# Optimization experiments

Measured on AMD Instinct MI355X. Metric: run time of the kernel, lower is better.

## Reference

```python
import jax, jax.numpy as jnp
import numpy as np
from jax import lax

D_MODEL = 1024
D_INNER = 2048   # expand * d_model
D_STATE = 16
D_CONV = 4
DT_RANK = 64     # ceil(d_model / 16)
B_SZ, L_SEQ = 2, 2048


def setup_inputs() -> dict:
    key = jax.random.key(0)
    ks = jax.random.split(key, 12)
    s = lambda *sh: 1.0 / np.sqrt(sh[-1])
    inp = {
        "x": jax.random.normal(ks[0], (B_SZ, L_SEQ, D_MODEL), jnp.float32),
        "in_proj_w": jax.random.normal(ks[1], (2 * D_INNER, D_MODEL), jnp.float32) * s(D_MODEL),
        "conv_w": jax.random.normal(ks[2], (D_INNER, 1, D_CONV), jnp.float32) * 0.3,
        "conv_b": jax.random.normal(ks[3], (D_INNER,), jnp.float32) * 0.05,
        "x_proj_w": jax.random.normal(ks[4], (DT_RANK + 2 * D_STATE, D_INNER), jnp.float32) * s(D_INNER),
        "dt_proj_w": jax.random.normal(ks[5], (D_INNER, DT_RANK), jnp.float32) * s(DT_RANK),
        "dt_proj_b": jnp.log(jnp.exp(jax.random.uniform(ks[6], (D_INNER,), jnp.float32, 1e-3, 1e-1)) - 1.0),
        "A_log": jnp.log(jnp.broadcast_to(jnp.arange(1, D_STATE + 1, dtype=jnp.float32), (D_INNER, D_STATE))),
        "D": jnp.ones((D_INNER,), jnp.float32),
        "out_proj_w": jax.random.normal(ks[7], (D_MODEL, D_INNER), jnp.float32) * s(D_INNER),
        "ln_w": jnp.ones((D_MODEL,), jnp.float32),
        "ln_b": jnp.zeros((D_MODEL,), jnp.float32),
    }
    return inp


def _mamba(x, in_proj_w, conv_w, conv_b, x_proj_w, dt_proj_w, dt_proj_b, A_log, D, out_proj_w):
    # x: [B, L, d_model]
    xz = x @ in_proj_w.T                             # [B, L, 2*d_inner]
    u, z = jnp.split(xz, 2, axis=-1)                 # [B, L, d_inner] each
    # depthwise causal conv1d along L
    u_c = jnp.swapaxes(u, 1, 2)                      # [B, d_inner, L]
    u_c = lax.conv_general_dilated(
        u_c, conv_w, window_strides=(1,), padding=[(D_CONV - 1, 0)],
        feature_group_count=D_INNER, dimension_numbers=("NCH", "OIH", "NCH"))
    u_c = u_c + conv_b[None, :, None]
    u_c = jax.nn.silu(jnp.swapaxes(u_c, 1, 2))       # [B, L, d_inner]
    # input-dependent dt, B, C
    x_dbl = u_c @ x_proj_w.T                         # [B, L, dt_rank + 2*d_state]
    dt_lr = x_dbl[..., :DT_RANK]
    Bm = x_dbl[..., DT_RANK:DT_RANK + D_STATE]       # [B, L, d_state]
    Cm = x_dbl[..., DT_RANK + D_STATE:]              # [B, L, d_state]
    dt = jax.nn.softplus(dt_lr @ dt_proj_w.T + dt_proj_b)  # [B, L, d_inner]
    A = -jnp.exp(A_log)                              # [d_inner, d_state]

    def step(h, inputs):
        dt_t, b_t, c_t, u_t = inputs                 # [B,d_inner],[B,N],[B,N],[B,d_inner]
        dA = jnp.exp(dt_t[:, :, None] * A)           # [B, d_inner, N]
        h = h * dA + (dt_t * u_t)[:, :, None] * b_t[:, None, :]
        y_t = jnp.einsum("bdn,bn->bd", h, c_t)
        return h, y_t

    h0 = jnp.zeros((x.shape[0], D_INNER, D_STATE), x.dtype)
    xs = (jnp.swapaxes(dt, 0, 1), jnp.swapaxes(Bm, 0, 1),
          jnp.swapaxes(Cm, 0, 1), jnp.swapaxes(u_c, 0, 1))
    _, ys = lax.scan(step, h0, xs)                   # ys: [L, B, d_inner]
    y = jnp.swapaxes(ys, 0, 1) + u_c * D             # skip connection D*u
    y = y * jax.nn.silu(z)                           # gate
    return y @ out_proj_w.T                          # [B, L, d_model]


def _layernorm(x, w, b, eps=1e-5):
    mu = jnp.mean(x, axis=-1, keepdims=True)
    var = jnp.mean(jnp.square(x - mu), axis=-1, keepdims=True)
    return (x - mu) * lax.rsqrt(var + eps) * w + b


def reference(x, in_proj_w, conv_w, conv_b, x_proj_w, dt_proj_w, dt_proj_b,
              A_log, D, out_proj_w, ln_w, ln_b):
    y = _mamba(x, in_proj_w, conv_w, conv_b, x_proj_w, dt_proj_w, dt_proj_b,
               A_log, D, out_proj_w)
    return _layernorm(y + x, ln_w, ln_b)  # dropout_level=0 -> identity
```

## Files before the change

### kernel.cpp

```cpp
#include <hip/hip_runtime.h>
#include <hip/hip_bf16.h>
#include <math.h>

#define DEV static __device__ __forceinline__

typedef __hip_bfloat16 bf16;
typedef __attribute__((ext_vector_type(8))) short bf16x8;
typedef __attribute__((ext_vector_type(4))) short bf16x4;
typedef __attribute__((ext_vector_type(4))) float f32x4;

static constexpr int D_MODEL = 1024;
static constexpr int D_INNER = 2048;
static constexpr int D_STATE = 16;
static constexpr int DT_RANK = 64;
static constexpr int B_SZ   = 2;
static constexpr int L_SEQ  = 2048;
static constexpr int T_TOK  = B_SZ * L_SEQ;
static constexpr int LC     = 64;
static constexpr int NC     = L_SEQ / LC;
static constexpr int NXP    = DT_RANK + 2 * D_STATE;
static constexpr int KSPLIT = 8;

static constexpr int P_CONVW = 0;
static constexpr int P_CONVB = 8192;
static constexpr int P_DTB   = 10240;
static constexpr int P_ALOG  = 12288;
static constexpr int P_DW    = 45056;
static constexpr int P_LNW   = 47104;
static constexpr int P_LNB   = 48128;
static constexpr int P_TOT   = 49152;

DEV float bf2f(bf16 x) { return __bfloat162float(x); }
DEV bf16  f2bf(float x) { return __float2bfloat16(x); }
DEV float sigmoidf_(float x) { return 1.0f / (1.0f + __expf(-x)); }
DEV float s2f(short s) { bf16 b; __builtin_memcpy(&b, &s, 2); return bf2f(b); }
DEV short f2s(float x) { bf16 b = f2bf(x); short s; __builtin_memcpy(&s, &b, 2); return s; }

DEV bool probe_f32(const unsigned short* probe) { return probe[1] == 0; }

DEV void async_copy16(const void* g, void* l) {
  __builtin_amdgcn_global_load_lds(
      (const __attribute__((address_space(1))) void*)g,
      (__attribute__((address_space(3))) void*)l, 16, 0, 0);
}

template <int N>
DEV void vm_wait() {
  if constexpr (N == 6) asm volatile("s_waitcnt vmcnt(6)" ::: "memory");
  else                  asm volatile("s_waitcnt vmcnt(0)" ::: "memory");
}

__global__ void cvt_all(const void* s0, const void* s1, const void* s2,
                        const void* s3, const void* s4,
                        const void* s5, const void* s6, const void* s7,
                        const void* s8, const void* s9, const void* s10,
                        const void* s11,
                        bf16* d0, bf16* d1, bf16* d2, bf16* d3, bf16* d4,
                        float* params,
                        const unsigned short* __restrict__ probe)
{
  long i = (long)(blockIdx.x * 256 + threadIdx.x) * 8;
  const void* src; long off;
  bf16* dstb = nullptr; float* dstf = nullptr;
  if      (i <  4194304) { src = s0;  dstb = d0; off = i; }
  else if (i <  8388608) { src = s1;  dstb = d1; off = i - 4194304; }
  else if (i <  8585216) { src = s2;  dstb = d2; off = i - 8388608; }
  else if (i <  8716288) { src = s3;  dstb = d3; off = i - 8585216; }
  else if (i < 10813440) { src = s4;  dstb = d4; off = i - 8716288; }
  else if (i < 10821632) { src = s5;  dstf = params + P_CONVW; off = i - 10813440; }
  else if (i < 10823680) { src = s6;  dstf = params + P_CONVB; off = i - 10821632; }
  else if (i < 10825728) { src = s7;  dstf = params + P_DTB;   off = i - 10823680; }
  else if (i < 10858496) { src = s8;  dstf = params + P_ALOG;  off = i - 10825728; }
  else if (i < 10860544) { src = s9;  dstf = params + P_DW;    off = i - 10858496; }
  else if (i < 10861568) { src = s10; dstf = params + P_LNW;   off = i - 10860544; }
  else if (i < 10862592) { src = s11; dstf = params + P_LNB;   off = i - 10861568; }
  else return;
  bool isf32 = probe_f32(probe);
  float v[8];
  if (isf32) {
    float4 a = *(const float4*)((const float*)src + off);
    float4 b = *(const float4*)((const float*)src + off + 4);
    v[0]=a.x; v[1]=a.y; v[2]=a.z; v[3]=a.w;
    v[4]=b.x; v[5]=b.y; v[6]=b.z; v[7]=b.w;
  } else {
    bf16x8 t = *(const bf16x8*)((const bf16*)src + off);
    #pragma unroll
    for (int k = 0; k < 8; ++k) { short sk = t[k]; v[k] = s2f(sk); }
  }
  if (dstb) {
    bf16x8 o;
    #pragma unroll
    for (int k = 0; k < 8; ++k) o[k] = f2s(v[k]);
    *(bf16x8*)(dstb + off) = o;
  } else {
    f32x4 a = {v[0], v[1], v[2], v[3]};
    f32x4 b = {v[4], v[5], v[6], v[7]};
    *(f32x4*)(dstf + off)     = a;
    *(f32x4*)(dstf + off + 4) = b;
  }
}

static constexpr int SLOT = 48 * 1024;
static constexpr int BOFF = 32 * 1024;

DEV void stage_A(const bf16* __restrict__ A, int ld, int bm, int k0,
                 char* slot, int tid) {
  #pragma unroll
  for (int j = 0; j < 4; ++j) {
    int p   = j * 8192 + tid * 16;
    int row = p >> 7;
    int ck  = ((p >> 4) & 7) ^ (row & 7);
    async_copy16(A + (size_t)(bm + row) * ld + k0 + ck * 8,
                 slot + j * 8192 + (tid >> 6) * 1024);
  }
}

DEV void stage_B(const bf16* __restrict__ B, int ld, int bn, int k0,
                 char* slot, int tid) {
  #pragma unroll
  for (int j = 0; j < 2; ++j) {
    int p   = j * 8192 + tid * 16;
    int row = p >> 7;
    int ck  = ((p >> 4) & 7) ^ (row & 7);
    async_copy16(B + (size_t)(bn + row) * ld + k0 + ck * 8,
                 slot + BOFF + j * 8192 + (tid >> 6) * 1024);
  }
}

template <int MODE>
DEV void gemm_pipe(const bf16* __restrict__ A, const bf16* __restrict__ B,
                   int M, int K, int ld,
                   void* __restrict__ o0, void* __restrict__ o1,
                   const float* __restrict__ cw, const float* __restrict__ cb)
{
  __shared__ __align__(16) char ring[3 * SLOT];
  const bf16* Aorig = A;
  const bf16* Borig = B;
  if (MODE == 3) {
    A += (size_t)blockIdx.z * K;
    B += (size_t)blockIdx.z * K;
  }
  const int tid  = threadIdx.x;
  const int wave = tid >> 6;
  const int lane = tid & 63;
  const int bm = blockIdx.x * 256;
  const int bn = blockIdx.y * 128;
  const int wm = (wave >> 1) * 64;
  const int wn = (wave & 1) * 64;
  const int fr = lane & 15;
  const int fq = lane >> 4;
  const int NT = K / 64;

  f32x4 acc[4][4];
  #pragma unroll
  for (int i = 0; i < 4; ++i)
    #pragma unroll
    for (int j = 0; j < 4; ++j)
      #pragma unroll
      for (int r = 0; r < 4; ++r) acc[i][j][r] = 0.0f;

  stage_A(A, ld, bm, 0,  ring,        tid);
  stage_B(B, ld, bn, 0,  ring,        tid);
  stage_A(A, ld, bm, 64, ring + SLOT, tid);
  stage_B(B, ld, bn, 64, ring + SLOT, tid);

  int scur = 0;
  #pragma unroll 1
  for (int tk = 0; tk < NT; ++tk) {
    if (tk < NT - 1) vm_wait<6>();
    else             vm_wait<0>();
    __builtin_amdgcn_sched_barrier(0);
    __builtin_amdgcn_s_barrier();
    __builtin_amdgcn_sched_barrier(0);

    const char* sa = ring + scur * SLOT;
    int snxt = scur + 2; if (snxt >= 3) snxt -= 3;
    char* sn = ring + snxt * SLOT;

    bf16x8 af[4][2], bg[2][2];
    #pragma unroll
    for (int mi = 0; mi < 4; ++mi)
      #pragma unroll
      for (int kk = 0; kk < 2; ++kk) {
        int row = wm + mi * 16 + fr;
        af[mi][kk] = *(const bf16x8*)(sa + row * 128 + (((kk * 4 + fq) ^ (fr & 7)) * 16));
      }
    #pragma unroll
    for (int ni = 0; ni < 2; ++ni)
      #pragma unroll
      for (int kk = 0; kk < 2; ++kk) {
        int row = wn + ni * 16 + fr;
        bg[ni][kk] = *(const bf16x8*)(sa + BOFF + row * 128 + (((kk * 4 + fq) ^ (fr & 7)) * 16));
      }
    __builtin_amdgcn_sched_barrier(0);
    if (tk + 2 < NT) stage_A(A, ld, bm, (tk + 2) * 64, sn, tid);
    __builtin_amdgcn_sched_barrier(0);
    asm volatile("s_waitcnt lgkmcnt(0)" ::: "memory");
    __builtin_amdgcn_sched_barrier(0);
    __builtin_amdgcn_s_setprio(1);
    #pragma unroll
    for (int kk = 0; kk < 2; ++kk)
      #pragma unroll
      for (int mi = 0; mi < 4; ++mi)
        #pragma unroll
        for (int ni = 0; ni < 2; ++ni)
          acc[mi][ni] = __builtin_amdgcn_mfma_f32_16x16x32_bf16(af[mi][kk], bg[ni][kk], acc[mi][ni], 0, 0, 0);
    __builtin_amdgcn_s_setprio(0);
    __builtin_amdgcn_sched_barrier(0);

    bf16x8 bh[2][2];
    #pragma unroll
    for (int ni = 0; ni < 2; ++ni)
      #pragma unroll
      for (int kk = 0; kk < 2; ++kk) {
        int row = wn + (ni + 2) * 16 + fr;
        bh[ni][kk] = *(const bf16x8*)(sa + BOFF + row * 128 + (((kk * 4 + fq) ^ (fr & 7)) * 16));
      }
    __builtin_amdgcn_sched_barrier(0);
    if (tk + 2 < NT) stage_B(B, ld, bn, (tk + 2) * 64, sn, tid);
    __builtin_amdgcn_sched_barrier(0);
    asm volatile("s_waitcnt lgkmcnt(0)" ::: "memory");
    __builtin_amdgcn_sched_barrier(0);
    __builtin_amdgcn_s_setprio(1);
    #pragma unroll
    for (int kk = 0; kk < 2; ++kk)
      #pragma unroll
      for (int mi = 0; mi < 4; ++mi)
        #pragma unroll
        for (int ni = 0; ni < 2; ++ni)
          acc[mi][ni + 2] = __builtin_amdgcn_mfma_f32_16x16x32_bf16(af[mi][kk], bh[ni][kk], acc[mi][ni + 2], 0, 0, 0);
    __builtin_amdgcn_s_setprio(0);
    __builtin_amdgcn_sched_barrier(0);

    scur = (scur + 1 == 3) ? 0 : scur + 1;
  }

  const int er = (lane >> 4) * 4;
  const int ec = lane & 15;

  if (MODE == 3) {
    #pragma unroll
    for (int mi = 0; mi < 4; ++mi)
      #pragma unroll
      for (int ni = 0; ni < 4; ++ni)
        #pragma unroll
        for (int r = 0; r < 4; ++r) {
          int row = bm + wm + mi * 16 + er + r;
          int col = bn + wn + ni * 16 + ec;
          ((bf16*)o0)[((size_t)blockIdx.z * M + row) * D_MODEL + col] = f2bf(acc[mi][ni][r]);
        }
    return;
  }

  if (bn >= D_INNER) {
    #pragma unroll
    for (int mi = 0; mi < 4; ++mi)
      #pragma unroll
      for (int ni = 0; ni < 4; ++ni)
        #pragma unroll
        for (int r = 0; r < 4; ++r) {
          int row = bm + wm + mi * 16 + er + r;
          int col = bn + wn + ni * 16 + ec - D_INNER;
          float v = acc[mi][ni][r];
          ((bf16*)o1)[(size_t)row * D_INNER + col] = f2bf(v * sigmoidf_(v));
        }
    return;
  }

  __syncthreads();
  bf16*  uT  = (bf16*)ring;
  float* cws = (float*)(ring + 70656);
  float* cbs = (float*)(ring + 72704);

  #pragma unroll
  for (int mi = 0; mi < 4; ++mi)
    #pragma unroll
    for (int ni = 0; ni < 4; ++ni)
      #pragma unroll
      for (int r = 0; r < 4; ++r)
        uT[(size_t)(wm + mi * 16 + er + r + 3) * 136 + wn + ni * 16 + ec] = f2bf(acc[mi][ni][r]);

  if (tid < 128) {
    *(f32x4*)(cws + tid * 4) = *(const f32x4*)(cw + (size_t)(bn + tid) * 4);
    cbs[tid] = cb[bn + tid];
  }

  if ((bm & (L_SEQ - 1)) != 0 && tid < 384) {
    int j = tid >> 7;
    int c = tid & 127;
    const bf16* xr = Aorig + (size_t)(bm - 3 + j) * ld;
    const bf16* wr = Borig + (size_t)(bn + c) * ld;
    float s = 0.0f;
    for (int k8 = 0; k8 < 1024; k8 += 8) {
      bf16x8 xa = *(const bf16x8*)(xr + k8);
      bf16x8 wb = *(const bf16x8*)(wr + k8);
      #pragma unroll
      for (int q = 0; q < 8; ++q) { short a = xa[q], b = wb[q]; s += s2f(a) * s2f(b); }
    }
    uT[(size_t)j * 136 + c] = f2bf(s);
  }
  __syncthreads();

  const int cg = tid & 15;
  float cwr[4][8], cbr[8];
  #pragma unroll
  for (int i = 0; i < 8; ++i) {
    f32x4 w4 = *(const f32x4*)(cws + (cg * 8 + i) * 4);
    cwr[0][i] = w4[0]; cwr[1][i] = w4[1]; cwr[2][i] = w4[2]; cwr[3][i] = w4[3];
    cbr[i] = cbs[cg * 8 + i];
  }
  const int lbase = bm & (L_SEQ - 1);
  #pragma unroll
  for (int j = 0; j < 8; ++j) {
    int row = (tid >> 4) + j * 32;
    float a8[8];
    #pragma unroll
    for (int i = 0; i < 8; ++i) a8[i] = cbr[i];
    #pragma unroll
    for (int w = 0; w < 4; ++w) {
      if (lbase + row - 3 + w >= 0) {
        bf16x8 u8 = *(const bf16x8*)(uT + (size_t)(row + w) * 136 + cg * 8);
        #pragma unroll
        for (int i = 0; i < 8; ++i) { short uu = u8[i]; a8[i] += s2f(uu) * cwr[w][i]; }
      }
    }
    bf16x8 o;
    #pragma unroll
    for (int i = 0; i < 8; ++i) o[i] = f2s(a8[i] * sigmoidf_(a8[i]));
    *(bf16x8*)((bf16*)o0 + (size_t)(bm + row) * D_INNER + bn + cg * 8) = o;
  }
}

__global__ void __launch_bounds__(256) k_xproj(const bf16* __restrict__ A,
                                               const bf16* __restrict__ B,
                                               float* __restrict__ o0)
{
  __shared__ __align__(16) bf16 As[128 * 32];
  __shared__ __align__(16) bf16 Bs[128 * 32];
  const int M = T_TOK, N = NXP, K = D_INNER / KSPLIT, ld = D_INNER;
  A += (size_t)blockIdx.z * K;
  B += (size_t)blockIdx.z * K;
  const int tid  = threadIdx.x;
  const int wave = tid >> 6;
  const int lane = tid & 63;
  const int bm = blockIdx.x * 128;
  const int bn = 0;
  const int wm = (wave >> 1) * 64;
  const int wn = (wave & 1) * 64;

  f32x4 acc[4][4];
  #pragma unroll
  for (int i = 0; i < 4; ++i)
    #pragma unroll
    for (int j = 0; j < 4; ++j)
      #pragma unroll
      for (int r = 0; r < 4; ++r) acc[i][j][r] = 0.0f;

  const int ar0 = tid >> 2;
  const int ar1 = ar0 + 64;
  const int ac  = (tid & 3) * 8;
  const int fr = lane & 15;
  const int fk = (lane >> 4) * 8;

  for (int k0 = 0; k0 < K; k0 += 32) {
    bf16x8 a0 = *(const bf16x8*)(A + (size_t)(bm + ar0) * ld + k0 + ac);
    bf16x8 a1 = *(const bf16x8*)(A + (size_t)(bm + ar1) * ld + k0 + ac);
    int r0 = bn + ar0; if (r0 > N - 1) r0 = N - 1;
    int r1 = bn + ar1; if (r1 > N - 1) r1 = N - 1;
    bf16x8 b0 = *(const bf16x8*)(B + (size_t)r0 * ld + k0 + ac);
    bf16x8 b1 = *(const bf16x8*)(B + (size_t)r1 * ld + k0 + ac);
    __syncthreads();
    *(bf16x8*)(As + ar0 * 32 + ac) = a0;
    *(bf16x8*)(As + ar1 * 32 + ac) = a1;
    *(bf16x8*)(Bs + ar0 * 32 + ac) = b0;
    *(bf16x8*)(Bs + ar1 * 32 + ac) = b1;
    __syncthreads();

    bf16x8 af[4], bg[4];
    #pragma unroll
    for (int mi = 0; mi < 4; ++mi)
      af[mi] = *(const bf16x8*)(As + (wm + mi * 16 + fr) * 32 + fk);
    #pragma unroll
    for (int ni = 0; ni < 4; ++ni)
      bg[ni] = *(const bf16x8*)(Bs + (wn + ni * 16 + fr) * 32 + fk);
    #pragma unroll
    for (int mi = 0; mi < 4; ++mi)
      #pragma unroll
      for (int ni = 0; ni < 4; ++ni)
        acc[mi][ni] = __builtin_amdgcn_mfma_f32_16x16x32_bf16(af[mi], bg[ni], acc[mi][ni], 0, 0, 0);
  }

  const int er = (lane >> 4) * 4;
  const int ec = lane & 15;
  #pragma unroll
  for (int mi = 0; mi < 4; ++mi)
    #pragma unroll
    for (int ni = 0; ni < 4; ++ni)
      #pragma unroll
      for (int r = 0; r < 4; ++r) {
        int row = bm + wm + mi * 16 + er + r;
        int col = bn + wn + ni * 16 + ec;
        if (col >= N) continue;
        o0[((size_t)blockIdx.z * M + row) * N + col] = acc[mi][ni][r];
      }
}

__global__ void __launch_bounds__(512) k_inproj(const bf16* A, const bf16* B,
    void* o0, void* o1, const float* cw, const float* cb) {
  gemm_pipe<0>(A, B, T_TOK, D_MODEL, D_MODEL, o0, o1, cw, cb);
}
__global__ void __launch_bounds__(512) k_outproj(const bf16* A, const bf16* B,
    void* o0) {
  gemm_pipe<3>(A, B, T_TOK, D_INNER / 2, D_INNER, o0, nullptr, nullptr, nullptr);
}

__global__ __launch_bounds__(256) void k_dtfuse(
    const float* __restrict__ partials,
    const bf16*  __restrict__ dtw,
    const float* __restrict__ dtbias,
    float* __restrict__ Bbuf, float* __restrict__ Cbuf,
    bf16* __restrict__ dtb)
{
  __shared__ __align__(16) bf16 Al[128 * 72];
  __shared__ __align__(16) bf16 Bl[128 * 72];
  const int tid = threadIdx.x;
  unsigned lin = blockIdx.x + gridDim.x * blockIdx.y;
  unsigned nid = (lin & 7) * 64 + (lin >> 3);
  const int cblk = nid & 15;
  const int tblk = nid >> 4;
  const int r0 = tblk * 128;
  const int c0 = cblk * 128;

  #pragma unroll
  for (int it = 0; it < 8; ++it) {
    int idx = it * 256 + tid;
    int row = idx >> 4;
    int g   = idx & 15;
    f32x4 s = {0.0f, 0.0f, 0.0f, 0.0f};
    #pragma unroll
    for (int kz = 0; kz < KSPLIT; ++kz)
      s += *(const f32x4*)(partials + ((size_t)kz * T_TOK + r0 + row) * NXP + g * 4);
    bf16x4 o;
    #pragma unroll
    for (int k = 0; k < 4; ++k) o[k] = f2s(s[k]);
    *(bf16x4*)(Al + row * 72 + g * 4) = o;
  }
  if (cblk == 0) {
    #pragma unroll
    for (int it = 0; it < 4; ++it) {
      int idx = it * 256 + tid;
      int row = idx >> 3;
      int g   = 16 + (idx & 7);
      f32x4 s = {0.0f, 0.0f, 0.0f, 0.0f};
      #pragma unroll
      for (int kz = 0; kz < KSPLIT; ++kz)
        s += *(const f32x4*)(partials + ((size_t)kz * T_TOK + r0 + row) * NXP + g * 4);
      if (g < 20) *(f32x4*)(Bbuf + (size_t)(r0 + row) * D_STATE + (g - 16) * 4) = s;
      else        *(f32x4*)(Cbuf + (size_t)(r0 + row) * D_STATE + (g - 20) * 4) = s;
    }
  }
  #pragma unroll
  for (int it = 0; it < 4; ++it) {
    int idx = it * 256 + tid;
    int row = idx >> 3;
    int cv  = (idx & 7) * 8;
    *(bf16x8*)(Bl + row * 72 + cv) = *(const bf16x8*)(dtw + (size_t)(c0 + row) * 64 + cv);
  }
  __syncthreads();

  const int wave = tid >> 6;
  const int lane = tid & 63;
  const int wm = (wave >> 1) * 64;
  const int wn = (wave & 1) * 64;
  const int fr = lane & 15;
  const int fk = (lane >> 4) * 8;
  const int er = (lane >> 4) * 4;
  const int ec = lane & 15;

  f32x4 acc[4][4];
  #pragma unroll
  for (int i = 0; i < 4; ++i)
    #pragma unroll
    for (int j = 0; j < 4; ++j)
      #pragma unroll
      for (int r = 0; r < 4; ++r) acc[i][j][r] = 0.0f;

  #pragma unroll
  for (int k0 = 0; k0 < 64; k0 += 32) {
    bf16x8 af[4], bg[4];
    #pragma unroll
    for (int mi = 0; mi < 4; ++mi)
      af[mi] = *(const bf16x8*)(Al + (wm + mi * 16 + fr) * 72 + k0 + fk);
    #pragma unroll
    for (int ni = 0; ni < 4; ++ni)
      bg[ni] = *(const bf16x8*)(Bl + (wn + ni * 16 + fr) * 72 + k0 + fk);
    #pragma unroll
    for (int mi = 0; mi < 4; ++mi)
      #pragma unroll
      for (int ni = 0; ni < 4; ++ni)
        acc[mi][ni] = __builtin_amdgcn_mfma_f32_16x16x32_bf16(af[mi], bg[ni], acc[mi][ni], 0, 0, 0);
  }

  #pragma unroll
  for (int mi = 0; mi < 4; ++mi)
    #pragma unroll
    for (int ni = 0; ni < 4; ++ni)
      #pragma unroll
      for (int r = 0; r < 4; ++r) {
        int orow = r0 + wm + mi * 16 + er + r;
        int ocol = c0 + wn + ni * 16 + ec;
        float v = acc[mi][ni][r] + dtbias[ocol];
        float sp = (v > 15.0f) ? v : __logf(1.0f + __expf(v));
        dtb[(size_t)orow * D_INNER + ocol] = f2bf(sp);
      }
}

DEV void load_Ad(const float* A_log, int d, float* Ad, bool& fast) {
  fast = true;
  #pragma unroll
  for (int n = 0; n < 16; ++n) {
    Ad[n] = -__expf(A_log[d * 16 + n]);
    fast = fast && (fabsf(Ad[n] + (float)(n + 1)) < 1e-3f * (n + 1));
  }
}
DEV void compute_decay(bool fast, float dtv, const float* Ad, float* dec) {
  if (fast) {
    float e1 = __expf(-dtv);
    float en = e1;
    #pragma unroll
    for (int n = 0; n < 16; ++n) { dec[n] = en; en *= e1; }
  } else {
    #pragma unroll
    for (int n = 0; n < 16; ++n) dec[n] = __expf(Ad[n] * dtv);
  }
}

__global__ __launch_bounds__(256) void scan_pass1(
    const bf16* __restrict__ dt, const bf16* __restrict__ uc_bf,
    const float* __restrict__ Bbuf, const float* __restrict__ A_log,
    float* __restrict__ hend, float* __restrict__ sumdt)
{
  __shared__ float Bs4[LC * D_STATE];
  __shared__ bf16 dts[16 * 256];
  __shared__ bf16 uts[16 * 256];
  int bid = blockIdx.x;
  int tid = threadIdx.x;
  int dt8 = bid & 7;
  int c = (bid >> 3) & (NC - 1);
  int b = bid >> 8;
  int d0 = dt8 * 256;
  int d  = d0 + tid;
  int t0g = b * L_SEQ + c * LC;

  ((f32x4*)Bs4)[tid] = ((const f32x4*)(Bbuf + (size_t)t0g * D_STATE))[tid];

  float Ad[16], h[16];
  bool fast;
  load_Ad(A_log, d, Ad, fast);
  #pragma unroll
  for (int n = 0; n < 16; ++n) h[n] = 0.0f;
  float sdt = 0.0f;

  for (int sub = 0; sub < 4; ++sub) {
    __syncthreads();
    #pragma unroll
    for (int rep = 0; rep < 2; ++rep) {
      int idx = rep * 256 + tid;
      int row = idx >> 5;
      int col = (idx & 31) * 8;
      size_t src = (size_t)(t0g + sub * 16 + row) * D_INNER + d0 + col;
      *(bf16x8*)(dts + row * 256 + col) = *(const bf16x8*)(dt + src);
      *(bf16x8*)(uts + row * 256 + col) = *(const bf16x8*)(uc_bf + src);
    }
    __syncthreads();
    for (int t = 0; t < 16; ++t) {
      float dtv = bf2f(dts[t * 256 + tid]);
      float uv  = bf2f(uts[t * 256 + tid]);
      float su  = dtv * uv;
      sdt += dtv;
      float dec[16];
      compute_decay(fast, dtv, Ad, dec);
      const float* Bp = Bs4 + (sub * 16 + t) * 16;
      #pragma unroll
      for (int n = 0; n < 16; ++n)
        h[n] = h[n] * dec[n] + su * Bp[n];
    }
  }
  size_t base = ((size_t)(b * NC + c) * D_INNER + d) * 16;
  #pragma unroll
  for (int q = 0; q < 4; ++q)
    *(f32x4*)(hend + base + q * 4) = *(f32x4*)(h + q * 4);
  sumdt[(size_t)(b * NC + c) * D_INNER + d] = sdt;
}

__global__ __launch_bounds__(256) void scan_pass2(
    float* __restrict__ hend, const float* __restrict__ sumdt,
    const float* __restrict__ A_log)
{
  __shared__ float Ms[4][64];
  __shared__ float Es[4][64];
  int bid = blockIdx.x;
  int tid = threadIdx.x;
  int cg   = tid >> 6;
  int lane = tid & 63;
  int dloc = lane >> 4;
  int n    = lane & 15;
  int b     = bid >> 9;
  int d     = (bid & 511) * 4 + dloc;

  float a = -__expf(A_log[d * 16 + n]);

  float Ml[8], El[8];
  float M = 1.0f, E = 0.0f;
  #pragma unroll
  for (int j = 0; j < 8; ++j) {
    int c = cg * 8 + j;
    size_t sbase = (size_t)(b * NC + c) * D_INNER + d;
    float m = __expf(a * sumdt[sbase]);
    float e = hend[sbase * 16 + n];
    Ml[j] = M; El[j] = E;
    M = m * M;
    E = m * E + e;
  }
  Ms[cg][lane] = M;
  Es[cg][lane] = E;
  __syncthreads();
  float Ep = 0.0f;
  for (int g = 0; g < cg; ++g) {
    float Mg = Ms[g][lane], Eg = Es[g][lane];
    Ep = Mg * Ep + Eg;
  }
  #pragma unroll
  for (int j = 0; j < 8; ++j) {
    int c = cg * 8 + j;
    size_t sbase = (size_t)(b * NC + c) * D_INNER + d;
    hend[sbase * 16 + n] = Ml[j] * Ep + El[j];
  }
}

__global__ __launch_bounds__(256) void scan_pass3(
    const bf16* __restrict__ dt, const bf16* __restrict__ uc_bf,
    const float* __restrict__ Bbuf, const float* __restrict__ Cbuf,
    const bf16* __restrict__ z_silu, const float* __restrict__ hstart,
    const float* __restrict__ A_log, const float* __restrict__ Dw,
    bf16* __restrict__ y_bf)
{
  __shared__ float Bs4[LC * D_STATE];
  __shared__ float Cs4[LC * D_STATE];
  __shared__ bf16 dts[16 * 256];
  __shared__ bf16 uts[16 * 256];
  __shared__ bf16 zts[16 * 256];
  int bid = blockIdx.x;
  int tid = threadIdx.x;
  int dt8 = bid & 7;
  int c = (bid >> 3) & (NC - 1);
  int b = bid >> 8;
  int d0 = dt8 * 256;
  int d  = d0 + tid;
  int t0g = b * L_SEQ + c * LC;

  ((f32x4*)Bs4)[tid] = ((const f32x4*)(Bbuf + (size_t)t0g * D_STATE))[tid];
  ((f32x4*)Cs4)[tid] = ((const f32x4*)(Cbuf + (size_t)t0g * D_STATE))[tid];

  float Ad[16], h[16];
  bool fast;
  load_Ad(A_log, d, Ad, fast);
  size_t base = ((size_t)(b * NC + c) * D_INNER + d) * 16;
  #pragma unroll
  for (int q = 0; q < 4; ++q)
    *(f32x4*)(h + q * 4) = *(const f32x4*)(hstart + base + q * 4);
  float Dv = Dw[d];

  for (int sub = 0; sub < 4; ++sub) {
    __syncthreads();
    #pragma unroll
    for (int rep = 0; rep < 2; ++rep) {
      int idx = rep * 256 + tid;
      int row = idx >> 5;
      int col = (idx & 31) * 8;
      size_t src = (size_t)(t0g + sub * 16 + row) * D_INNER + d0 + col;
      *(bf16x8*)(dts + row * 256 + col) = *(const bf16x8*)(dt + src);
      *(bf16x8*)(uts + row * 256 + col) = *(const bf16x8*)(uc_bf + src);
      *(bf16x8*)(zts + row * 256 + col) = *(const bf16x8*)(z_silu + src);
    }
    __syncthreads();
    for (int t = 0; t < 16; ++t) {
      float dtv = bf2f(dts[t * 256 + tid]);
      float uv  = bf2f(uts[t * 256 + tid]);
      float zv  = bf2f(zts[t * 256 + tid]);
      float su  = dtv * uv;
      float dec[16];
      compute_decay(fast, dtv, Ad, dec);
      const float* Bp = Bs4 + (sub * 16 + t) * 16;
      const float* Cp = Cs4 + (sub * 16 + t) * 16;
      float y = 0.0f;
      #pragma unroll
      for (int n = 0; n < 16; ++n) {
        h[n] = h[n] * dec[n] + su * Bp[n];
        y += h[n] * Cp[n];
      }
      y = (y + uv * Dv) * zv;
      y_bf[(size_t)(t0g + sub * 16 + t) * D_INNER + d] = f2bf(y);
    }
  }
}

__global__ void ln_kernel(const bf16* __restrict__ parts,
                          const bf16* __restrict__ x_bf,
                          const float* __restrict__ w,
                          const float* __restrict__ bia,
                          void* __restrict__ out,
                          const unsigned short* __restrict__ probe)
{
  int t = blockIdx.x;
  int tid = threadIdx.x;
  const bf16* p0 = parts + (size_t)t * D_MODEL;
  const bf16* p1 = parts + ((size_t)T_TOK + t) * D_MODEL;
  const bf16* xr = x_bf + (size_t)t * D_MODEL;
  float v[4];
  float s = 0.0f, q = 0.0f;
  #pragma unroll
  for (int k = 0; k < 4; ++k) {
    int col = tid + k * 256;
    v[k] = bf2f(p0[col]) + bf2f(p1[col]) + bf2f(xr[col]);
    s += v[k]; q += v[k] * v[k];
  }
  #pragma unroll
  for (int off = 32; off >= 1; off >>= 1) {
    s += __shfl_down(s, off);
    q += __shfl_down(q, off);
  }
  __shared__ float red[8];
  __shared__ float mv[2];
  int wave = tid >> 6, lane = tid & 63;
  if (lane == 0) { red[wave] = s; red[4 + wave] = q; }
  __syncthreads();
  if (tid == 0) {
    float S = red[0] + red[1] + red[2] + red[3];
    float Q = red[4] + red[5] + red[6] + red[7];
    float mu = S * (1.0f / D_MODEL);
    float var = Q * (1.0f / D_MODEL) - mu * mu;
    mv[0] = mu; mv[1] = rsqrtf(var + 1e-5f);
  }
  __syncthreads();
  float mu = mv[0], rs = mv[1];
  bool isf32 = probe_f32(probe);
  #pragma unroll
  for (int k = 0; k < 4; ++k) {
    int col = tid + k * 256;
    float r = (v[k] - mu) * rs * w[col] + bia[col];
    if (isf32) ((float*)out)[(size_t)t * D_MODEL + col] = r;
    else       ((bf16*) out)[(size_t)t * D_MODEL + col] = f2bf(r);
  }
}

extern "C" void kernel_launch(void* const* d_in, const int* in_sizes, int n_in,
                              void* d_out, int out_size, void* d_ws, size_t ws_size,
                              hipStream_t stream)
{
  const void* x        = d_in[0];
  const void* in_w     = d_in[1];
  const void* conv_w   = d_in[2];
  const void* conv_b   = d_in[3];
  const void* xproj_w  = d_in[4];
  const void* dtproj_w = d_in[5];
  const void* dtproj_b = d_in[6];
  const void* A_log    = d_in[7];
  const void* Dw       = d_in[8];
  const void* out_w    = d_in[9];
  const void* ln_w     = d_in[10];
  const void* ln_b     = d_in[11];
  const unsigned short* probe = (const unsigned short*)A_log;

  char* p = (char*)d_ws;
  auto alloc = [&](size_t bytes) { char* r = p; p += (bytes + 255) & ~255ull; return r; };
  bf16*  x_bf   = (bf16*) alloc((size_t)T_TOK * D_MODEL * 2);
  bf16*  inw_bf = (bf16*) alloc((size_t)2 * D_INNER * D_MODEL * 2);
  bf16*  xpw_bf = (bf16*) alloc((size_t)NXP * D_INNER * 2);
  bf16*  dtw_bf = (bf16*) alloc((size_t)D_INNER * DT_RANK * 2);
  bf16*  outw_bf= (bf16*) alloc((size_t)D_MODEL * D_INNER * 2);
  float* params = (float*)alloc((size_t)P_TOT * 4);
  bf16*  scratch= (bf16*) alloc((size_t)T_TOK * D_INNER * 2);
  bf16*  z_silu = (bf16*) alloc((size_t)T_TOK * D_INNER * 2);
  bf16*  uc_bf  = (bf16*) alloc((size_t)T_TOK * D_INNER * 2);
  float* Bbuf   = (float*)alloc((size_t)T_TOK * D_STATE * 4);
  float* Cbuf   = (float*)alloc((size_t)T_TOK * D_STATE * 4);
  bf16*  dtb    = (bf16*) alloc((size_t)T_TOK * D_INNER * 2);
  float* hend   = (float*)alloc((size_t)B_SZ * NC * D_INNER * 16 * 4);
  float* sumdt  = (float*)alloc((size_t)B_SZ * NC * D_INNER * 4);
  float* xparts = (float*)scratch;
  bf16*  y_bf   = scratch;
  bf16*  oparts = z_silu;

  dim3 blk(256);
  dim3 blk512(512);
  cvt_all<<<5304, blk, 0, stream>>>(x, in_w, xproj_w, dtproj_w, out_w,
                                    conv_w, conv_b, dtproj_b, A_log, Dw, ln_w, ln_b,
                                    x_bf, inw_bf, xpw_bf, dtw_bf, outw_bf, params, probe);

  k_inproj<<<dim3(T_TOK / 256, (2 * D_INNER) / 128), blk512, 0, stream>>>(
      x_bf, inw_bf, uc_bf, z_silu, params + P_CONVW, params + P_CONVB);
  k_xproj<<<dim3(T_TOK / 128, 1, KSPLIT), blk, 0, stream>>>(uc_bf, xpw_bf, xparts);
  k_dtfuse<<<dim3(16, 32), blk, 0, stream>>>(xparts, dtw_bf, params + P_DTB, Bbuf, Cbuf, dtb);
  scan_pass1<<<B_SZ * NC * (D_INNER / 256), blk, 0, stream>>>(dtb, uc_bf, Bbuf, params + P_ALOG, hend, sumdt);
  scan_pass2<<<(B_SZ * D_INNER) / 2, blk, 0, stream>>>(hend, sumdt, params + P_ALOG);
  scan_pass3<<<B_SZ * NC * (D_INNER / 256), blk, 0, stream>>>(
      dtb, uc_bf, Bbuf, Cbuf, z_silu, hend, params + P_ALOG, params + P_DW, y_bf);
  k_outproj<<<dim3(T_TOK / 256, D_MODEL / 128, 2), blk512, 0, stream>>>(y_bf, outw_bf, oparts);
  ln_kernel<<<T_TOK, blk, 0, stream>>>(oparts, x_bf, params + P_LNW, params + P_LNB, d_out, probe);
}
```

Before: 294.6 us.

## Replace in-GEMM halo recomputation with cross-tile boundary exchange and fixup kernel

Before, each in_proj tile recomputed the three preceding token rows of u with a scalar 1024-long dot product, so the depthwise conv had its causal halo. That serial per-thread loop ran in the GEMM epilogue. Now each tile writes its first and last three u rows to small global buffers and skips the first three conv outputs. A new small kernel then recomputes those boundary conv outputs from the neighbouring tiles' rows. This removes the slow scalar halo work from the GEMM, at the cost of one extra tiny kernel launch and its dependency.

```diff
diff --git a/kernel.cpp b/kernel.cpp
--- a/kernel.cpp
+++ b/kernel.cpp
@@ -131,11 +131,10 @@
 DEV void gemm_pipe(const bf16* __restrict__ A, const bf16* __restrict__ B,
                    int M, int K, int ld,
                    void* __restrict__ o0, void* __restrict__ o1,
-                   const float* __restrict__ cw, const float* __restrict__ cb)
+                   const float* __restrict__ cw, const float* __restrict__ cb,
+                   bf16* __restrict__ ufirst, bf16* __restrict__ ulast)
 {
   __shared__ __align__(16) char ring[3 * SLOT];
-  const bf16* Aorig = A;
-  const bf16* Borig = B;
   if (MODE == 3) {
     A += (size_t)blockIdx.z * K;
     B += (size_t)blockIdx.z * K;
@@ -278,28 +277,21 @@
     for (int ni = 0; ni < 4; ++ni)
       #pragma unroll
       for (int r = 0; r < 4; ++r)
-        uT[(size_t)(wm + mi * 16 + er + r + 3) * 136 + wn + ni * 16 + ec] = f2bf(acc[mi][ni][r]);
+        uT[(size_t)(wm + mi * 16 + er + r) * 136 + wn + ni * 16 + ec] = f2bf(acc[mi][ni][r]);
 
   if (tid < 128) {
     *(f32x4*)(cws + tid * 4) = *(const f32x4*)(cw + (size_t)(bn + tid) * 4);
     cbs[tid] = cb[bn + tid];
   }
-
-  if ((bm & (L_SEQ - 1)) != 0 && tid < 384) {
-    int j = tid >> 7;
-    int c = tid & 127;
-    const bf16* xr = Aorig + (size_t)(bm - 3 + j) * ld;
-    const bf16* wr = Borig + (size_t)(bn + c) * ld;
-    float s = 0.0f;
-    for (int k8 = 0; k8 < 1024; k8 += 8) {
-      bf16x8 xa = *(const bf16x8*)(xr + k8);
-      bf16x8 wb = *(const bf16x8*)(wr + k8);
-      #pragma unroll
-      for (int q = 0; q < 8; ++q) { short a = xa[q], b = wb[q]; s += s2f(a) * s2f(b); }
-    }
-    uT[(size_t)j * 136 + c] = f2bf(s);
-  }
   __syncthreads();
+
+  if (tid < 48) {
+    int i  = tid >> 4;
+    int c8 = (tid & 15) * 8;
+    size_t hb = ((size_t)(bm >> 8) * 3 + i) * D_INNER + bn + c8;
+    *(bf16x8*)(ufirst + hb) = *(const bf16x8*)(uT + (size_t)i * 136 + c8);
+    *(bf16x8*)(ulast  + hb) = *(const bf16x8*)(uT + (size_t)(253 + i) * 136 + c8);
+  }
 
   const int cg = tid & 15;
   float cwr[4][8], cbr[8];
@@ -313,13 +305,14 @@
   #pragma unroll
   for (int j = 0; j < 8; ++j) {
     int row = (tid >> 4) + j * 32;
+    if (row < 3 && lbase != 0) continue;
     float a8[8];
     #pragma unroll
     for (int i = 0; i < 8; ++i) a8[i] = cbr[i];
     #pragma unroll
     for (int w = 0; w < 4; ++w) {
-      if (lbase + row - 3 + w >= 0) {
-        bf16x8 u8 = *(const bf16x8*)(uT + (size_t)(row + w) * 136 + cg * 8);
+      if (row - 3 + w >= 0) {
+        bf16x8 u8 = *(const bf16x8*)(uT + (size_t)(row - 3 + w) * 136 + cg * 8);
         #pragma unroll
         for (int i = 0; i < 8; ++i) { short uu = u8[i]; a8[i] += s2f(uu) * cwr[w][i]; }
       }
@@ -329,6 +322,41 @@
     for (int i = 0; i < 8; ++i) o[i] = f2s(a8[i] * sigmoidf_(a8[i]));
     *(bf16x8*)((bf16*)o0 + (size_t)(bm + row) * D_INNER + bn + cg * 8) = o;
   }
+}
+
+__global__ void __launch_bounds__(256) k_convfix(
+    const bf16* __restrict__ ufirst, const bf16* __restrict__ ulast,
+    const float* __restrict__ cw, const float* __restrict__ cb,
+    bf16* __restrict__ uc_bf)
+{
+  int idx = blockIdx.x * 256 + threadIdx.x;
+  int e4 = idx * 4;
+  int ti = e4 >> 11;
+  int c4 = e4 & 2047;
+  int tb = ti / 3, r = ti - tb * 3;
+  int rb = (tb < 7) ? tb + 1 : tb + 2;
+  int token = rb * 256 + r;
+  float a[4];
+  float4 wv[4];
+  #pragma unroll
+  for (int i = 0; i < 4; ++i) {
+    a[i]  = cb[c4 + i];
+    wv[i] = *(const float4*)(cw + (size_t)(c4 + i) * 4);
+  }
+  #pragma unroll
+  for (int w = 0; w < 4; ++w) {
+    int g = r - 3 + w;
+    const bf16* srcrow = (g < 0)
+        ? (ulast  + ((size_t)(rb - 1) * 3 + (g + 3)) * D_INNER)
+        : (ufirst + ((size_t)rb * 3 + g) * D_INNER);
+    bf16x4 u = *(const bf16x4*)(srcrow + c4);
+    #pragma unroll
+    for (int i = 0; i < 4; ++i) { short su = u[i]; a[i] += s2f(su) * ((const float*)&wv[i])[w]; }
+  }
+  bf16x4 o;
+  #pragma unroll
+  for (int i = 0; i < 4; ++i) o[i] = f2s(a[i] * sigmoidf_(a[i]));
+  *(bf16x4*)(uc_bf + (size_t)token * D_INNER + c4) = o;
 }
 
 __global__ void __launch_bounds__(256) k_xproj(const bf16* __restrict__ A,
@@ -406,12 +434,14 @@
 }
 
 __global__ void __launch_bounds__(512) k_inproj(const bf16* A, const bf16* B,
-    void* o0, void* o1, const float* cw, const float* cb) {
-  gemm_pipe<0>(A, B, T_TOK, D_MODEL, D_MODEL, o0, o1, cw, cb);
+    void* o0, void* o1, const float* cw, const float* cb,
+    bf16* ufirst, bf16* ulast) {
+  gemm_pipe<0>(A, B, T_TOK, D_MODEL, D_MODEL, o0, o1, cw, cb, ufirst, ulast);
 }
 __global__ void __launch_bounds__(512) k_outproj(const bf16* A, const bf16* B,
     void* o0) {
-  gemm_pipe<3>(A, B, T_TOK, D_INNER / 2, D_INNER, o0, nullptr, nullptr, nullptr);
+  gemm_pipe<3>(A, B, T_TOK, D_INNER / 2, D_INNER, o0, nullptr, nullptr, nullptr,
+               nullptr, nullptr);
 }
 
 __global__ __launch_bounds__(256) void k_dtfuse(
@@ -788,6 +818,8 @@
   bf16*  dtb    = (bf16*) alloc((size_t)T_TOK * D_INNER * 2);
   float* hend   = (float*)alloc((size_t)B_SZ * NC * D_INNER * 16 * 4);
   float* sumdt  = (float*)alloc((size_t)B_SZ * NC * D_INNER * 4);
+  bf16*  ufirst = (bf16*) alloc((size_t)16 * 3 * D_INNER * 2);
+  bf16*  ulast  = (bf16*) alloc((size_t)16 * 3 * D_INNER * 2);
   float* xparts = (float*)scratch;
   bf16*  y_bf   = scratch;
   bf16*  oparts = z_silu;
@@ -799,7 +831,8 @@
                                     x_bf, inw_bf, xpw_bf, dtw_bf, outw_bf, params, probe);
 
   k_inproj<<<dim3(T_TOK / 256, (2 * D_INNER) / 128), blk512, 0, stream>>>(
-      x_bf, inw_bf, uc_bf, z_silu, params + P_CONVW, params + P_CONVB);
+      x_bf, inw_bf, uc_bf, z_silu, params + P_CONVW, params + P_CONVB, ufirst, ulast);
+  k_convfix<<<84, blk, 0, stream>>>(ufirst, ulast, params + P_CONVW, params + P_CONVB, uc_bf);
   k_xproj<<<dim3(T_TOK / 128, 1, KSPLIT), blk, 0, stream>>>(uc_bf, xpw_bf, xparts);
   k_dtfuse<<<dim3(16, 32), blk, 0, stream>>>(xparts, dtw_bf, params + P_DTB, Bbuf, Cbuf, dtb);
   scan_pass1<<<B_SZ * NC * (D_INNER / 256), blk, 0, stream>>>(dtb, uc_bf, Bbuf, params + P_ALOG, hend, sumdt);
```

New measurement: 268.0 us, median of 3. -9.0%, faster.
